# Kernel tuning notes

Hardware: AMD Instinct MI355X
Metric: run time of the kernel (lower is better)

## Reference

```python
import jax, jax.numpy as jnp
import numpy as np

OUT = 7          # output_size
NS = 2           # roi_align_num_samples -> 14x14 sampling grid
S = OUT * NS
SCALES = (0.25, 0.125, 0.0625, 0.03125)
IMG = 1024.0
NUM_LEVELS = 4


def setup_inputs() -> dict:
    key = jax.random.key(0)
    ks = jax.random.split(key, 5)
    shapes = [(2, 256, 256, 256), (2, 256, 128, 128), (2, 256, 64, 64), (2, 256, 32, 32)]
    inp = {}
    for i, (k, s) in enumerate(zip(ks[:4], shapes)):
        inp[f"feat{i}"] = jax.random.normal(k, s, dtype=jnp.float32)
    B, N = 2, 512
    u = jax.random.uniform(ks[4], (B, N, 4), dtype=jnp.float32)
    x1 = u[..., 0] * (IMG - 64.0)
    y1 = u[..., 1] * (IMG - 64.0)
    w = 32.0 + u[..., 2] * 640.0
    h = 32.0 + u[..., 3] * 640.0
    x2 = jnp.minimum(x1 + w, IMG - 1.0)
    y2 = jnp.minimum(y1 + h, IMG - 1.0)
    inp["proposals"] = jnp.stack([x1, y1, x2, y2], axis=-1)  # [B,N,4]
    return inp


def _levels(proposals):
    # proposals: [B,N,4]
    pw = proposals[..., 2] - proposals[..., 0]
    ph = proposals[..., 3] - proposals[..., 1]
    areas = pw * ph
    lvl = jnp.floor(2.0 + jnp.log2(jnp.sqrt(areas) / 224.0))
    return jnp.clip(lvl, 0, 3).astype(jnp.int32)  # [B,N]


def _sampling_grid(prop):
    # prop: [N,4] already scaled to feature coords -> x,y each [N,S,S]
    w_unit = (prop[:, 2] - prop[:, 0]) / S   # [N]
    h_unit = (prop[:, 3] - prop[:, 1]) / S
    r = jnp.arange(S, dtype=prop.dtype)
    wr = r[None, :] * w_unit[:, None] + w_unit[:, None] * 0.5 + prop[:, 0:1]  # [N,S]
    hr = r[None, :] * h_unit[:, None] + h_unit[:, None] * 0.5 + prop[:, 1:2]  # [N,S]
    x = jnp.broadcast_to(wr[:, None, :], (prop.shape[0], S, S))  # varies along last axis
    y = jnp.broadcast_to(hr[:, :, None], (prop.shape[0], S, S))  # varies along middle axis
    return x, y


def _bilinear(feat, x, y):
    # feat: [C,H,W]; x,y: [N,S,S] -> [N,C,S,S]
    H, W = feat.shape[1], feat.shape[2]
    x0 = jnp.floor(x).astype(jnp.int32); x1 = x0 + 1
    y0 = jnp.floor(y).astype(jnp.int32); y1 = y0 + 1
    xc = jnp.clip(x, 0.0, W - 1); x0 = jnp.clip(x0, 0, W - 1); x1 = jnp.clip(x1, 0, W - 1)
    yc = jnp.clip(y, 0.0, H - 1); y0 = jnp.clip(y0, 0, H - 1); y1 = jnp.clip(y1, 0, H - 1)
    la = feat[:, y0, x0]  # [C,N,S,S]
    lb = feat[:, y1, x0]
    lc = feat[:, y0, x1]
    ld = feat[:, y1, x1]
    x0f = x0.astype(xc.dtype); x1f = x1.astype(xc.dtype)
    y0f = y0.astype(yc.dtype); y1f = y1.astype(yc.dtype)
    wa = jax.lax.stop_gradient((x1f - xc) * (y1f - yc))
    wb = jax.lax.stop_gradient((x1f - xc) * (yc - y0f))
    wc = jax.lax.stop_gradient((xc - x0f) * (y1f - yc))
    wd = jax.lax.stop_gradient((xc - x0f) * (yc - y0f))
    out = wa[None] * la + wb[None] * lb + wc[None] * lc + wd[None] * ld  # [C,N,S,S]
    return jnp.transpose(out, (1, 0, 2, 3))


def _adaptive_max_pool(x):
    # [N,C,S,S] -> [N,C,OUT,OUT]  (S = 2*OUT, so 2x2 max blocks)
    N, C = x.shape[0], x.shape[1]
    return x.reshape(N, C, OUT, NS, OUT, NS).max(axis=(3, 5))


def reference(feat0, feat1, feat2, feat3, proposals):
    feats = (feat0, feat1, feat2, feat3)
    B, N = proposals.shape[0], proposals.shape[1]
    C = feats[0].shape[1]
    levels = _levels(proposals)  # [B,N]
    out = jnp.zeros((B, N, C, OUT, OUT), dtype=feats[0].dtype)

    def per_image(feat, prop):
        x, y = _sampling_grid(prop)
        return _adaptive_max_pool(_bilinear(feat, x, y))  # [N,C,OUT,OUT]

    for i in range(NUM_LEVELS):
        scaled = proposals * SCALES[i]  # [B,N,4]
        pooled = jax.vmap(per_image)(feats[i], scaled)  # [B,N,C,OUT,OUT]
        mask = (levels == i).astype(pooled.dtype)[:, :, None, None, None]
        out = out + mask * pooled
    return out.reshape(B * N, C, OUT, OUT)
```

## Files before the change

### kernel.cpp

```cpp
#include <hip/hip_runtime.h>
#include <math.h>


#define CSPLIT 4
#define CPB (256 / CSPLIT)

__global__ __launch_bounds__(256) void roialign_chan_kernel(
    const float* __restrict__ f0, const float* __restrict__ f1,
    const float* __restrict__ f2, const float* __restrict__ f3,
    const float* __restrict__ props, float* __restrict__ out)
{
    const int blk = blockIdx.x;
    const int cs  = blk & (CSPLIT - 1);
    const int n   = blk >> 2;
    const int b   = n >> 9;

    const int tid = threadIdx.x;
    const int sx  = tid & 15;
    const int sy  = tid >> 4;
    const float rx = (float)min(sx, 13);
    const float ry = (float)min(sy, 13);

    const float px1 = props[n * 4 + 0];
    const float py1 = props[n * 4 + 1];
    const float px2 = props[n * 4 + 2];
    const float py2 = props[n * 4 + 3];
    const float area = (px2 - px1) * (py2 - py1);
    float lf = floorf(2.0f + log2f(sqrtf(area) / 224.0f));
    lf = fminf(fmaxf(lf, 0.0f), 3.0f);
    const int lvl = (int)lf;

    const float* feat;
    int W;
    float scale;
    if (lvl == 0)      { feat = f0; W = 256; scale = 0.25f;    }
    else if (lvl == 1) { feat = f1; W = 128; scale = 0.125f;   }
    else if (lvl == 2) { feat = f2; W = 64;  scale = 0.0625f;  }
    else               { feat = f3; W = 32;  scale = 0.03125f; }

    const float sx1f = px1 * scale;
    const float sy1f = py1 * scale;
    const float sx2f = px2 * scale;
    const float sy2f = py2 * scale;
    const float w_unit = (sx2f - sx1f) / 14.0f;
    const float h_unit = (sy2f - sy1f) / 14.0f;
    const float Wm1 = (float)(W - 1);

    const float fx = rx * w_unit + w_unit * 0.5f + sx1f;
    int x0 = (int)floorf(fx);
    const float xc = fminf(fmaxf(fx, 0.0f), Wm1);
    int x0c = min(max(x0, 0), W - 1);
    int x1c = min(max(x0 + 1, 0), W - 1);
    const float wx0 = (float)x1c - xc;
    const float wx1 = xc - (float)x0c;
    const int xv = min(x0c, W - 2);

    const float fy = ry * h_unit + h_unit * 0.5f + sy1f;
    int y0 = (int)floorf(fy);
    const float yc = fminf(fmaxf(fy, 0.0f), Wm1);
    int y0c = min(max(y0, 0), W - 1);
    int y1c = min(max(y0 + 1, 0), W - 1);
    const float wy0 = (float)y1c - yc;
    const float wy1 = yc - (float)y0c;

    const int off00 = y0c * W + xv;
    const int off10 = y1c * W + xv;
    const int WW = W * W;

    const int c0 = cs * CPB;
    const float* fb = feat + ((size_t)b * 256 + (size_t)c0) * (size_t)WW;

    const bool active = (((sx | sy) & 1) == 0) && sx < 14 && sy < 14;
    float* outp = out + (size_t)(n * 256 + c0) * 49
                      + (size_t)(sy >> 1) * 7 + (size_t)(sx >> 1);

    #pragma unroll 4
    for (int c = 0; c < CPB; ++c) {
        const float* p = fb + (size_t)c * (size_t)WW;
        const float2 a = *reinterpret_cast<const float2*>(p + off00);
        const float2 bb = *reinterpret_cast<const float2*>(p + off10);

        float v = wy0 * (wx0 * a.x + wx1 * a.y)
                + wy1 * (wx0 * bb.x + wx1 * bb.y);

        v = fmaxf(v, __shfl_xor(v, 1));
        v = fmaxf(v, __shfl_xor(v, 16));

        if (active) outp[(size_t)c * 49] = v;
    }
}

extern "C" void kernel_launch(void* const* d_in, const int* in_sizes, int n_in,
                              void* d_out, int out_size, void* d_ws, size_t ws_size,
                              hipStream_t stream) {
    const float* f0 = (const float*)d_in[0];
    const float* f1 = (const float*)d_in[1];
    const float* f2 = (const float*)d_in[2];
    const float* f3 = (const float*)d_in[3];
    const float* props = (const float*)d_in[4];
    float* out = (float*)d_out;

    dim3 grid(1024 * CSPLIT), block(256);
    hipLaunchKernelGGL(roialign_chan_kernel, grid, block, 0, stream,
                       f0, f1, f2, f3, props, out);
}
```

Baseline: 75.26 us.

## Stage ROI feature window rows in shared memory before bilinear sampling

When the sampled window of an ROI fits in 32x32, the block cooperatively loads that window for four channels at a time into shared memory, then does the bilinear interpolation and 2x2 max from LDS. Larger windows fall back to the original direct float2 gathers. The aim is to replace scattered global gathers with coalesced row loads. In exchange it adds barriers, loads unused window pixels, and uses 16 KB of LDS per block.

```diff
diff --git a/kernel.cpp b/kernel.cpp
--- a/kernel.cpp
+++ b/kernel.cpp
@@ -4,20 +4,25 @@
 
 #define CSPLIT 4
 #define CPB (256 / CSPLIT)
+#define WROW 33
+#define CHSLOT (32 * WROW)
 
-__global__ __launch_bounds__(256) void roialign_chan_kernel(
+__global__ __launch_bounds__(256) void roialign_rowstage_kernel(
     const float* __restrict__ f0, const float* __restrict__ f1,
     const float* __restrict__ f2, const float* __restrict__ f3,
     const float* __restrict__ props, float* __restrict__ out)
 {
+    __shared__ float S[4 * CHSLOT];
+
     const int blk = blockIdx.x;
     const int cs  = blk & (CSPLIT - 1);
     const int n   = blk >> 2;
     const int b   = n >> 9;
 
-    const int tid = threadIdx.x;
-    const int sx  = tid & 15;
-    const int sy  = tid >> 4;
+    const int tid  = threadIdx.x;
+    const int lane = tid & 63;
+    const int sx   = tid & 15;
+    const int sy   = tid >> 4;
     const float rx = (float)min(sx, 13);
     const float ry = (float)min(sy, 13);
 
@@ -63,10 +68,19 @@
     const float wy0 = (float)y1c - yc;
     const float wy1 = yc - (float)y0c;
 
-    const int off00 = y0c * W + xv;
-    const int off10 = y1c * W + xv;
+    const float fx_0  = 0.0f  * w_unit + w_unit * 0.5f + sx1f;
+    const float fx_13 = 13.0f * w_unit + w_unit * 0.5f + sx1f;
+    const int xv0  = min(min(max((int)floorf(fx_0),  0), W - 1), W - 2);
+    const int xv13 = min(min(max((int)floorf(fx_13), 0), W - 1), W - 2);
+    const int w_win = xv13 - xv0 + 2;
+    const float fy_0  = 0.0f  * h_unit + h_unit * 0.5f + sy1f;
+    const float fy_13 = 13.0f * h_unit + h_unit * 0.5f + sy1f;
+    const int ymin = min(max((int)floorf(fy_0), 0), W - 1);
+    const int ymax = min(max((int)floorf(fy_13) + 1, 0), W - 1);
+    const int h_win = ymax - ymin + 1;
+    const bool stageable = (w_win <= 32) && (h_win <= 32);
+
     const int WW = W * W;
-
     const int c0 = cs * CPB;
     const float* fb = feat + ((size_t)b * 256 + (size_t)c0) * (size_t)WW;
 
@@ -74,19 +88,53 @@
     float* outp = out + (size_t)(n * 256 + c0) * 49
                       + (size_t)(sy >> 1) * 7 + (size_t)(sx >> 1);
 
-    #pragma unroll 4
-    for (int c = 0; c < CPB; ++c) {
-        const float* p = fb + (size_t)c * (size_t)WW;
-        const float2 a = *reinterpret_cast<const float2*>(p + off00);
-        const float2 bb = *reinterpret_cast<const float2*>(p + off10);
+    if (stageable) {
+        const int loff00 = (y0c - ymin) * WROW + (xv - xv0);
+        const int loff10 = (y1c - ymin) * WROW + (xv - xv0);
+        const int ch_s = tid >> 6;
+        const int r_half = lane >> 5;
+        const int col = lane & 31;
+        const int col_g = min(xv0 + col, W - 1);
+        const float* fwin = fb + (size_t)ymin * (size_t)W;
 
-        float v = wy0 * (wx0 * a.x + wx1 * a.y)
-                + wy1 * (wx0 * bb.x + wx1 * bb.y);
+        for (int cb = 0; cb < CPB; cb += 4) {
+            {
+                const float* src = fwin + (size_t)(cb + ch_s) * (size_t)WW;
+                float* dst = S + ch_s * CHSLOT;
+                for (int r = r_half; r < h_win; r += 2)
+                    dst[r * WROW + col] = src[(size_t)r * (size_t)W + col_g];
+            }
+            __syncthreads();
 
-        v = fmaxf(v, __shfl_xor(v, 1));
-        v = fmaxf(v, __shfl_xor(v, 16));
-
-        if (active) outp[(size_t)c * 49] = v;
+            #pragma unroll
+            for (int j = 0; j < 4; ++j) {
+                const int base = j * CHSLOT;
+                const float a0 = S[base + loff00];
+                const float a1 = S[base + loff00 + 1];
+                const float b0 = S[base + loff10];
+                const float b1 = S[base + loff10 + 1];
+                float v = wy0 * (wx0 * a0 + wx1 * a1)
+                        + wy1 * (wx0 * b0 + wx1 * b1);
+                v = fmaxf(v, __shfl_xor(v, 1));
+                v = fmaxf(v, __shfl_xor(v, 16));
+                if (active) outp[(size_t)(cb + j) * 49] = v;
+            }
+            __syncthreads();
+        }
+    } else {
+        const int off00 = y0c * W + xv;
+        const int off10 = y1c * W + xv;
+        #pragma unroll 4
+        for (int c = 0; c < CPB; ++c) {
+            const float* p = fb + (size_t)c * (size_t)WW;
+            const float2 a  = *reinterpret_cast<const float2*>(p + off00);
+            const float2 bb = *reinterpret_cast<const float2*>(p + off10);
+            float v = wy0 * (wx0 * a.x  + wx1 * a.y)
+                    + wy1 * (wx0 * bb.x + wx1 * bb.y);
+            v = fmaxf(v, __shfl_xor(v, 1));
+            v = fmaxf(v, __shfl_xor(v, 16));
+            if (active) outp[(size_t)c * 49] = v;
+        }
     }
 }
 
@@ -101,6 +149,6 @@
     float* out = (float*)d_out;
 
     dim3 grid(1024 * CSPLIT), block(256);
-    hipLaunchKernelGGL(roialign_chan_kernel, grid, block, 0, stream,
+    hipLaunchKernelGGL(roialign_rowstage_kernel, grid, block, 0, stream,
                        f0, f1, f2, f3, props, out);
 }
```

New measurement: 94.21 us. 1.25x slower.
